# Kernel tuning notes

Measured on AMD Instinct MI355X. Metric: run time of the kernel, lower is better.

Reference implementation:

```python
import jax, jax.numpy as jnp
import numpy as np

B, CIN, H, W = 16, 1024, 32, 32
WIDTH = 256          # bottleneck width = planes * base_width/64 * cardinality
OUT = 1024           # planes * expansion
HEADS = WIDTH // 8   # 32
KS = 3               # kernel_size of SelfAttLayer


def unfold3x3(x):
    # x: (B, C, H, W) -> (B, C, 9, H, W), torch.nn.Unfold(3, padding=1) ordering (row-major kernel)
    xp = jnp.pad(x, ((0, 0), (0, 0), (1, 1), (1, 1)))
    h, w = x.shape[2], x.shape[3]
    patches = [xp[:, :, i:i + h, j:j + w] for i in range(KS) for j in range(KS)]
    return jnp.stack(patches, axis=2)


def bn(x, s, b):
    # inference-mode BatchNorm2d with running stats folded into per-channel scale/bias
    return x * s[None, :, None, None] + b[None, :, None, None]


def conv1x1(x, w):
    # w: (Cout, Cin)
    return jnp.einsum('bchw,oc->bohw', x, w)


def setup_inputs() -> dict:
    key = jax.random.key(0)
    ks = jax.random.split(key, 16)
    f = lambda k, shp, scale: (jax.random.normal(k, shp, dtype=jnp.float32) * scale)
    inp = {
        'x': f(ks[0], (B, CIN, H, W), 1.0),
        'w_conv1': f(ks[1], (WIDTH, CIN), 1.0 / np.sqrt(CIN)),
        'bn1_s': jnp.ones((WIDTH,), jnp.float32), 'bn1_b': jnp.zeros((WIDTH,), jnp.float32),
        'wq': f(ks[2], (WIDTH, WIDTH), 1.0 / np.sqrt(WIDTH)),
        'bnq_s': jnp.ones((WIDTH,), jnp.float32), 'bnq_b': jnp.zeros((WIDTH,), jnp.float32),
        'wk': f(ks[3], (WIDTH, WIDTH), 1.0 / np.sqrt(WIDTH)),
        'bnk_s': jnp.ones((WIDTH,), jnp.float32), 'bnk_b': jnp.zeros((WIDTH,), jnp.float32),
        'wv': f(ks[4], (WIDTH, WIDTH), 1.0 / np.sqrt(WIDTH)),
        'bnv_s': jnp.ones((WIDTH,), jnp.float32), 'bnv_b': jnp.zeros((WIDTH,), jnp.float32),
        'pos_h': f(ks[5], (WIDTH, KS, 1), 1.0),
        'pos_w': f(ks[6], (WIDTH, 1, KS), 1.0),
        'bnatt_s': jnp.ones((WIDTH,), jnp.float32), 'bnatt_b': jnp.zeros((WIDTH,), jnp.float32),
        'w_conv3': f(ks[7], (OUT, WIDTH), 1.0 / np.sqrt(WIDTH)),
        'bn3_s': jnp.ones((OUT,), jnp.float32), 'bn3_b': jnp.zeros((OUT,), jnp.float32),
    }
    return inp


def self_att(x, wq, bnq_s, bnq_b, wk, bnk_s, bnk_b, wv, bnv_s, bnv_b,
             pos_h, pos_w, bnatt_s, bnatt_b):
    b, c, h, w = x.shape
    d = c // HEADS
    q = jax.nn.relu(bn(conv1x1(x, wq), bnq_s, bnq_b))          # (B,C,H,W)
    k = jax.nn.relu(bn(conv1x1(x, wk), bnk_s, bnk_b))          # key_ks=1 -> 1x1 conv
    v = bn(conv1x1(x, wv), bnv_s, bnv_b)
    unfold_k = unfold3x3(k)                                     # (B,C,9,H,W)
    pos = (pos_h + pos_w).reshape(1, c, KS * KS, 1, 1)          # (1,C,9,1,1)
    kp = (unfold_k + pos).reshape(b, HEADS, d, KS * KS, h, w)
    qh = q.reshape(b, HEADS, d, h, w)
    attn = jnp.einsum('bgdhw,bgdkhw->bgkhw', qh, kp)            # (B,heads,9,H,W)
    attn = jax.nn.softmax(attn, axis=2)
    # local conv: each channel-group of size d shares its head's attention weights
    v_unf = unfold3x3(v).reshape(b, HEADS, d, KS * KS, h, w)
    out = jnp.einsum('bgdkhw,bgkhw->bgdhw', v_unf, attn).reshape(b, c, h, w)
    return jax.nn.relu(bn(out, bnatt_s, bnatt_b))


def reference(x, w_conv1, bn1_s, bn1_b, wq, bnq_s, bnq_b, wk, bnk_s, bnk_b,
              wv, bnv_s, bnv_b, pos_h, pos_w, bnatt_s, bnatt_b,
              w_conv3, bn3_s, bn3_b):
    residual = x
    h = jax.nn.relu(bn(conv1x1(x, w_conv1), bn1_s, bn1_b))
    h = self_att(h, wq, bnq_s, bnq_b, wk, bnk_s, bnk_b, wv, bnv_s, bnv_b,
                 pos_h, pos_w, bnatt_s, bnatt_b)
    h = bn(conv1x1(h, w_conv3), bn3_s, bn3_b)
    return jax.nn.relu(h + residual)
```

## Files before the change

### kernel.cpp

```cpp
#include <hip/hip_runtime.h>
#include <stdint.h>


typedef __attribute__((ext_vector_type(4))) float f32x4;
typedef __attribute__((ext_vector_type(8))) __bf16 bf16x8;
typedef __attribute__((ext_vector_type(4))) unsigned short u16x4;
typedef __attribute__((ext_vector_type(8))) unsigned short u16x8;

__device__ __forceinline__ float bf2f(unsigned short u) {
  union { unsigned int i; float f; } c; c.i = ((unsigned int)u) << 16; return c.f;
}
__device__ __forceinline__ unsigned short f2bf(float f) {
  union { float f; unsigned int i; } c; c.f = f;
  unsigned int x = c.i;
  return (unsigned short)((x + 0x7FFFu + ((x >> 16) & 1u)) >> 16);
}

__global__ __launch_bounds__(256) void k_transpose_x(const float* __restrict__ x,
                                                     unsigned short* __restrict__ xt) {
  __shared__ float tile[32][33];
  const int b  = blockIdx.z;
  const int c0 = blockIdx.y * 32;
  const int p0 = blockIdx.x * 32;
  const int tx = threadIdx.x & 31;
  const int ty = threadIdx.x >> 5;
  const float* xb = x + (size_t)b * 1048576;
  unsigned short* xtb = xt + (size_t)b * 1048576;
#pragma unroll
  for (int i = 0; i < 4; ++i)
    tile[ty + i * 8][tx] = xb[(size_t)(c0 + ty + i * 8) * 1024 + p0 + tx];
  __syncthreads();
#pragma unroll
  for (int i = 0; i < 4; ++i)
    xtb[(size_t)(p0 + ty + i * 8) * 1024 + c0 + tx] = f2bf(tile[tx][ty + i * 8]);
}

__global__ __launch_bounds__(256, 4) void k_gemm_stream(
    const float* __restrict__ A, const unsigned short* __restrict__ B,
    unsigned short* __restrict__ Cout, const float* __restrict__ scale,
    const float* __restrict__ bias, int K) {
  __shared__ unsigned short lA[2][64 * 32];
  __shared__ unsigned short lB[2][64 * 32];
  const int m0  = blockIdx.y * 64;
  const int n0  = blockIdx.x * 64;
  const int tid = threadIdx.x;
  const int lane = tid & 63;
  const int wid  = tid >> 6;
  const int wm = (wid >> 1) * 32, wn = (wid & 1) * 32;
  const int fr = lane & 15, fq = lane >> 4;

  f32x4 acc[2][2] = {};

  const int r = tid >> 2;
  const int g = tid & 3;
  const float*          Ag = A + (size_t)(m0 + r) * K + g * 8;
  const unsigned short* Bg = B + (size_t)(n0 + r) * K + g * 8;
  const int lofs = r * 32 + (g ^ (r & 3)) * 8;

  f32x4 aA[2], aB[2];
  u16x8 bvA, bvB;
  aA[0] = *(const f32x4*)(Ag);      aA[1] = *(const f32x4*)(Ag + 4);
  bvA   = *(const u16x8*)(Bg);
  aB[0] = *(const f32x4*)(Ag + 32); aB[1] = *(const f32x4*)(Ag + 36);
  bvB   = *(const u16x8*)(Bg + 32);

  int p = 0;
  for (int k0 = 0; k0 < K; k0 += 32, p ^= 1) {
    u16x8 ap;
#pragma unroll
    for (int i = 0; i < 8; ++i) ap[i] = f2bf(aA[i >> 2][i & 3]);
    *(u16x8*)&lA[p][lofs] = ap;
    *(u16x8*)&lB[p][lofs] = bvA;
    aA[0] = aB[0]; aA[1] = aB[1]; bvA = bvB;
    if (k0 + 64 < K) {
      aB[0] = *(const f32x4*)(Ag + k0 + 64);
      aB[1] = *(const f32x4*)(Ag + k0 + 68);
      bvB   = *(const u16x8*)(Bg + k0 + 64);
    }
    __syncthreads();

    bf16x8 af[2], bb[2];
#pragma unroll
    for (int i = 0; i < 2; ++i) {
      const int row = wm + i * 16 + fr;
      af[i] = *(const bf16x8*)&lA[p][row * 32 + (fq ^ (row & 3)) * 8];
    }
#pragma unroll
    for (int j = 0; j < 2; ++j) {
      const int row = wn + j * 16 + fr;
      bb[j] = *(const bf16x8*)&lB[p][row * 32 + (fq ^ (row & 3)) * 8];
    }
#pragma unroll
    for (int i = 0; i < 2; ++i)
#pragma unroll
      for (int j = 0; j < 2; ++j)
        acc[i][j] = __builtin_amdgcn_mfma_f32_16x16x32_bf16(af[i], bb[j], acc[i][j], 0, 0, 0);
  }

#pragma unroll
  for (int i = 0; i < 2; ++i) {
    const int ob = m0 + wm + i * 16 + fq * 4;
    const f32x4 s4 = *(const f32x4*)&scale[ob];
    const f32x4 b4 = *(const f32x4*)&bias[ob];
#pragma unroll
    for (int j = 0; j < 2; ++j) {
      const int P = n0 + wn + j * 16 + fr;
      u16x4 pk;
#pragma unroll
      for (int rr = 0; rr < 4; ++rr) {
        float v = fmaxf(acc[i][j][rr] * s4[rr] + b4[rr], 0.0f);
        pk[rr] = f2bf(v);
      }
      *(u16x4*)&Cout[(size_t)P * 256 + ob] = pk;
    }
  }
}

template <int MODE, int NT>
__global__ __launch_bounds__(256, 4) void k_gemm_k256(
    const float* __restrict__ A0, const float* __restrict__ A1,
    const float* __restrict__ A2, const unsigned short* __restrict__ B,
    void* __restrict__ CoutV,
    const float* __restrict__ s0, const float* __restrict__ s1,
    const float* __restrict__ s2, const float* __restrict__ b0,
    const float* __restrict__ b1, const float* __restrict__ b2,
    const float* __restrict__ resid) {
  __shared__ unsigned short lA[64 * 256];
  __shared__ unsigned short lB[2][64 * 32];
  const int mt = blockIdx.y;
  int seg, m_loc, do_relu;
  const float *A, *sc, *bi;
  if (MODE == 0) {
    seg = mt >> 2; m_loc = (mt & 3) * 64;
    A  = seg == 0 ? A0 : (seg == 1 ? A1 : A2);
    sc = seg == 0 ? s0 : (seg == 1 ? s1 : s2);
    bi = seg == 0 ? b0 : (seg == 1 ? b1 : b2);
    do_relu = (seg < 2);
  } else {
    seg = 0; m_loc = mt * 64; A = A0; sc = s0; bi = b0; do_relu = 1;
  }
  const int tid = threadIdx.x;
  const int lane = tid & 63, wid = tid >> 6;
  const int wm = (wid >> 1) * 32, wn = (wid & 1) * 32;
  const int fr = lane & 15, fq = lane >> 4;

  {
    const int rA = tid >> 2, qd = tid & 3;
    const float* Ag = A + (size_t)(m_loc + rA) * 256 + qd * 64;
#pragma unroll
    for (int m = 0; m < 8; ++m) {
      f32x4 lo = *(const f32x4*)(Ag + m * 8);
      f32x4 hi = *(const f32x4*)(Ag + m * 8 + 4);
      u16x8 pk;
#pragma unroll
      for (int e = 0; e < 4; ++e) pk[e] = f2bf(lo[e]);
#pragma unroll
      for (int e = 0; e < 4; ++e) pk[4 + e] = f2bf(hi[e]);
      const int cg = qd * 8 + m;
      *(u16x8*)&lA[rA * 256 + (cg ^ ((rA & 7) << 2)) * 8] = pk;
    }
  }

  const int rB = tid >> 2, gB = tid & 3;
  const int lofsB = rB * 32 + (gB ^ (rB & 3)) * 8;
  const int n0_blk = blockIdx.x * NT * 64;
  const unsigned short* Bg = B + (size_t)(n0_blk + rB) * 256 + gB * 8;

  u16x8 bvA = *(const u16x8*)(Bg);
  u16x8 bvB = *(const u16x8*)(Bg + 32);
  f32x4 acc[2][2] = {};
  float rres[2][2][4];
  int p = 0;
  const int TOT = NT * 8;

  for (int s = 0; s < TOT; ++s) {
    const int k0 = (s & 7) * 32;

    if (MODE == 1 && (s & 7) == 0) {
      const int n0 = n0_blk + (s >> 3) * 64;
#pragma unroll
      for (int i = 0; i < 2; ++i) {
        const int ol = m_loc + wm + i * 16 + fq * 4;
#pragma unroll
        for (int j = 0; j < 2; ++j) {
          const int P = n0 + wn + j * 16 + fr;
          const size_t base = (size_t)(P >> 10) * 1048576 + (size_t)(P & 1023);
#pragma unroll
          for (int rr = 0; rr < 4; ++rr)
            rres[i][j][rr] = resid[base + (size_t)(ol + rr) * 1024];
        }
      }
    }

    *(u16x8*)&lB[p][lofsB] = bvA;
    bvA = bvB;
    if (s + 2 < TOT) {
      const int s2i = s + 2;
      bvB = *(const u16x8*)(Bg + (size_t)(s2i >> 3) * 16384 + (s2i & 7) * 32);
    }
    __syncthreads();

    bf16x8 af[2], bb[2];
#pragma unroll
    for (int i = 0; i < 2; ++i) {
      const int row = wm + i * 16 + fr;
      const int cg = (k0 >> 3) + fq;
      af[i] = *(const bf16x8*)&lA[row * 256 + (cg ^ ((row & 7) << 2)) * 8];
    }
#pragma unroll
    for (int j = 0; j < 2; ++j) {
      const int row = wn + j * 16 + fr;
      bb[j] = *(const bf16x8*)&lB[p][row * 32 + (fq ^ (row & 3)) * 8];
    }
#pragma unroll
    for (int i = 0; i < 2; ++i)
#pragma unroll
      for (int j = 0; j < 2; ++j)
        acc[i][j] = __builtin_amdgcn_mfma_f32_16x16x32_bf16(af[i], bb[j], acc[i][j], 0, 0, 0);
    p ^= 1;

    if ((s & 7) == 7) {
      const int n0 = n0_blk + (s >> 3) * 64;
#pragma unroll
      for (int i = 0; i < 2; ++i) {
        const int ol = m_loc + wm + i * 16 + fq * 4;
        const f32x4 s4 = *(const f32x4*)&sc[ol];
        const f32x4 b4 = *(const f32x4*)&bi[ol];
#pragma unroll
        for (int j = 0; j < 2; ++j) {
          const int P = n0 + wn + j * 16 + fr;
          if (MODE == 0) {
            unsigned short* Cout = (unsigned short*)CoutV + (size_t)seg * 4194304;
            u16x4 pk;
#pragma unroll
            for (int rr = 0; rr < 4; ++rr) {
              float v = acc[i][j][rr] * s4[rr] + b4[rr];
              if (do_relu) v = fmaxf(v, 0.0f);
              pk[rr] = f2bf(v);
            }
            *(u16x4*)&Cout[(size_t)P * 256 + ol] = pk;
          } else {
            float* Cout = (float*)CoutV;
            const size_t base = (size_t)(P >> 10) * 1048576 + (size_t)(P & 1023);
#pragma unroll
            for (int rr = 0; rr < 4; ++rr) {
              float v = acc[i][j][rr] * s4[rr] + b4[rr] + rres[i][j][rr];
              Cout[base + (size_t)(ol + rr) * 1024] = fmaxf(v, 0.0f);
            }
          }
          acc[i][j] = (f32x4){0.f, 0.f, 0.f, 0.f};
        }
      }
    }
  }
}

__global__ __launch_bounds__(256, 4) void k_attn(
    const unsigned short* __restrict__ Q, const unsigned short* __restrict__ Kb,
    const unsigned short* __restrict__ Vb, unsigned short* __restrict__ O,
    const float* __restrict__ pos_h, const float* __restrict__ pos_w,
    const float* __restrict__ bs, const float* __restrict__ bb) {
  __shared__ float ph_l[3][256];
  __shared__ float pw_l[3][256];
  {
    const int c = threadIdx.x;
#pragma unroll
    for (int i = 0; i < 3; ++i) {
      ph_l[i][c] = pos_h[c * 3 + i];
      pw_l[i][c] = pos_w[c * 3 + i];
    }
  }
  __syncthreads();
  const int tid = threadIdx.x;
  const int g = tid & 31, s = tid >> 5;
  const int P = blockIdx.x * 8 + s;
  const int b = P >> 10, pix = P & 1023;
  const int hh = pix >> 5, ww = pix & 31;
  const int c0 = g * 8;

  float qf[8];
  {
    u16x8 qv = *(const u16x8*)&Q[(size_t)P * 256 + c0];
#pragma unroll
    for (int d = 0; d < 8; ++d) qf[d] = bf2f(qv[d]);
  }
  float Ai[3], Bj[3];
#pragma unroll
  for (int i = 0; i < 3; ++i) {
    float a = 0.f, w = 0.f;
#pragma unroll
    for (int d = 0; d < 8; ++d) {
      a += qf[d] * ph_l[i][c0 + d];
      w += qf[d] * pw_l[i][c0 + d];
    }
    Ai[i] = a; Bj[i] = w;
  }

  float S[9];
  int nPs[9];
#pragma unroll
  for (int t = 0; t < 9; ++t) {
    const int di = t / 3, dj = t % 3;
    const int nh = hh + di - 1, nw = ww + dj - 1;
    float sum = Ai[di] + Bj[dj];
    int nP = -1;
    if ((unsigned)nh < 32u && (unsigned)nw < 32u) {
      nP = (b << 10) + (nh << 5) + nw;
      u16x8 kv = *(const u16x8*)&Kb[(size_t)nP * 256 + c0];
#pragma unroll
      for (int d = 0; d < 8; ++d) sum += qf[d] * bf2f(kv[d]);
    }
    nPs[t] = nP;
    S[t] = sum;
  }

  float mx = S[0];
#pragma unroll
  for (int t = 1; t < 9; ++t) mx = fmaxf(mx, S[t]);
  float e[9], tot = 0.f;
#pragma unroll
  for (int t = 0; t < 9; ++t) { e[t] = __expf(S[t] - mx); tot += e[t]; }
  const float inv = 1.0f / tot;

  float of[8] = {0.f, 0.f, 0.f, 0.f, 0.f, 0.f, 0.f, 0.f};
#pragma unroll
  for (int t = 0; t < 9; ++t) {
    if (nPs[t] >= 0) {
      u16x8 vv = *(const u16x8*)&Vb[(size_t)nPs[t] * 256 + c0];
      const float w = e[t] * inv;
#pragma unroll
      for (int d = 0; d < 8; ++d) of[d] += w * bf2f(vv[d]);
    }
  }

  u16x8 res;
#pragma unroll
  for (int d = 0; d < 8; ++d) {
    float v = of[d] * bs[c0 + d] + bb[c0 + d];
    v = fmaxf(v, 0.0f);
    res[d] = f2bf(v);
  }
  *(u16x8*)&O[(size_t)P * 256 + c0] = res;
}

extern "C" void kernel_launch(void* const* d_in, const int* in_sizes, int n_in,
                              void* d_out, int out_size, void* d_ws, size_t ws_size,
                              hipStream_t stream) {
  (void)in_sizes; (void)n_in; (void)out_size; (void)ws_size;
  const float* x       = (const float*)d_in[0];
  const float* w1      = (const float*)d_in[1];
  const float* bn1_s   = (const float*)d_in[2];
  const float* bn1_b   = (const float*)d_in[3];
  const float* wq      = (const float*)d_in[4];
  const float* bnq_s   = (const float*)d_in[5];
  const float* bnq_b   = (const float*)d_in[6];
  const float* wk      = (const float*)d_in[7];
  const float* bnk_s   = (const float*)d_in[8];
  const float* bnk_b   = (const float*)d_in[9];
  const float* wv      = (const float*)d_in[10];
  const float* bnv_s   = (const float*)d_in[11];
  const float* bnv_b   = (const float*)d_in[12];
  const float* pos_h   = (const float*)d_in[13];
  const float* pos_w   = (const float*)d_in[14];
  const float* bnatt_s = (const float*)d_in[15];
  const float* bnatt_b = (const float*)d_in[16];
  const float* w3      = (const float*)d_in[17];
  const float* bn3_s   = (const float*)d_in[18];
  const float* bn3_b   = (const float*)d_in[19];

  char* ws = (char*)d_ws;
  unsigned short* h1t = (unsigned short*)(ws);
  unsigned short* qt  = (unsigned short*)(ws + 8388608);
  unsigned short* att = h1t;
  unsigned short* xt  = (unsigned short*)d_out;

  k_transpose_x<<<dim3(32, 32, 16), dim3(256), 0, stream>>>(x, xt);

  k_gemm_stream<<<dim3(256, 4), dim3(256), 0, stream>>>(w1, xt, h1t, bn1_s, bn1_b, 1024);

  k_gemm_k256<0, 4><<<dim3(64, 12), dim3(256), 0, stream>>>(
      wq, wk, wv, h1t, qt, bnq_s, bnk_s, bnv_s, bnq_b, bnk_b, bnv_b, nullptr);

  k_attn<<<dim3(2048), dim3(256), 0, stream>>>(qt, qt + 4194304, qt + 8388608, att,
                                               pos_h, pos_w, bnatt_s, bnatt_b);

  k_gemm_k256<1, 4><<<dim3(64, 16), dim3(256), 0, stream>>>(
      w3, nullptr, nullptr, att, d_out, bn3_s, nullptr, nullptr, bn3_b, nullptr,
      nullptr, x);
}
```

Before: 114.1 us.

## Fuse input transpose into conv1 GEMM with full-M tiles per block

Removes the separate x transpose/bf16 conversion kernel and has the conv1 GEMM read fp32 x directly from NCHW layout, transposing and converting it into LDS on the fly. Each block now computes all 256 output channels for 32 pixels (512 blocks), so x is read exactly once rather than written and reread as bf16. In exchange the weight matrix is reconverted from fp32 by every block, LDS stores of B are scattered 16-bit writes, and occupancy is lowered to 2 blocks per SIMD group with larger accumulators.

Measured after the change: 139.1 us. 21.9% more time.

```diff
diff --git a/kernel.cpp b/kernel.cpp
--- a/kernel.cpp
+++ b/kernel.cpp
@@ -16,102 +16,86 @@
   return (unsigned short)((x + 0x7FFFu + ((x >> 16) & 1u)) >> 16);
 }
 
-__global__ __launch_bounds__(256) void k_transpose_x(const float* __restrict__ x,
-                                                     unsigned short* __restrict__ xt) {
-  __shared__ float tile[32][33];
-  const int b  = blockIdx.z;
-  const int c0 = blockIdx.y * 32;
-  const int p0 = blockIdx.x * 32;
-  const int tx = threadIdx.x & 31;
-  const int ty = threadIdx.x >> 5;
-  const float* xb = x + (size_t)b * 1048576;
-  unsigned short* xtb = xt + (size_t)b * 1048576;
-#pragma unroll
-  for (int i = 0; i < 4; ++i)
-    tile[ty + i * 8][tx] = xb[(size_t)(c0 + ty + i * 8) * 1024 + p0 + tx];
-  __syncthreads();
-#pragma unroll
-  for (int i = 0; i < 4; ++i)
-    xtb[(size_t)(p0 + ty + i * 8) * 1024 + c0 + tx] = f2bf(tile[tx][ty + i * 8]);
-}
-
-__global__ __launch_bounds__(256, 4) void k_gemm_stream(
-    const float* __restrict__ A, const unsigned short* __restrict__ B,
-    unsigned short* __restrict__ Cout, const float* __restrict__ scale,
-    const float* __restrict__ bias, int K) {
-  __shared__ unsigned short lA[2][64 * 32];
-  __shared__ unsigned short lB[2][64 * 32];
-  const int m0  = blockIdx.y * 64;
-  const int n0  = blockIdx.x * 64;
+__global__ __launch_bounds__(256, 2) void k_conv1_fused(
+    const float* __restrict__ x, const float* __restrict__ W,
+    unsigned short* __restrict__ H, const float* __restrict__ scale,
+    const float* __restrict__ bias) {
+  __shared__ unsigned short lA[2][256 * 32];
+  __shared__ unsigned short lB[2][32 * 32];
+  const int n0 = blockIdx.x * 32;
   const int tid = threadIdx.x;
-  const int lane = tid & 63;
-  const int wid  = tid >> 6;
-  const int wm = (wid >> 1) * 32, wn = (wid & 1) * 32;
+  const int lane = tid & 63, wid = tid >> 6;
+  const int wm = wid * 64;
   const int fr = lane & 15, fq = lane >> 4;
 
-  f32x4 acc[2][2] = {};
-
-  const int r = tid >> 2;
-  const int g = tid & 3;
-  const float*          Ag = A + (size_t)(m0 + r) * K + g * 8;
-  const unsigned short* Bg = B + (size_t)(n0 + r) * K + g * 8;
-  const int lofs = r * 32 + (g ^ (r & 3)) * 8;
-
-  f32x4 aA[2], aB[2];
-  u16x8 bvA, bvB;
-  aA[0] = *(const f32x4*)(Ag);      aA[1] = *(const f32x4*)(Ag + 4);
-  bvA   = *(const u16x8*)(Bg);
-  aB[0] = *(const f32x4*)(Ag + 32); aB[1] = *(const f32x4*)(Ag + 36);
-  bvB   = *(const u16x8*)(Bg + 32);
+  f32x4 acc[4][2] = {};
+
+  const float* Ag = W + (size_t)tid * 1024;
+  const int tc = tid >> 3, tpp = (tid & 7) * 4;
+  const size_t xbase = (size_t)(n0 >> 10) * 1048576 + (n0 & 1023);
+
+  f32x4 aw[8];
+  f32x4 bx;
+#pragma unroll
+  for (int g = 0; g < 8; ++g) aw[g] = *(const f32x4*)(Ag + g * 4);
+  bx = *(const f32x4*)&x[xbase + (size_t)tc * 1024 + tpp];
 
   int p = 0;
-  for (int k0 = 0; k0 < K; k0 += 32, p ^= 1) {
-    u16x8 ap;
-#pragma unroll
-    for (int i = 0; i < 8; ++i) ap[i] = f2bf(aA[i >> 2][i & 3]);
-    *(u16x8*)&lA[p][lofs] = ap;
-    *(u16x8*)&lB[p][lofs] = bvA;
-    aA[0] = aB[0]; aA[1] = aB[1]; bvA = bvB;
-    if (k0 + 64 < K) {
-      aB[0] = *(const f32x4*)(Ag + k0 + 64);
-      aB[1] = *(const f32x4*)(Ag + k0 + 68);
-      bvB   = *(const u16x8*)(Bg + k0 + 64);
+  for (int k0 = 0; k0 < 1024; k0 += 32, p ^= 1) {
+#pragma unroll
+    for (int g = 0; g < 4; ++g) {
+      u16x8 pk;
+#pragma unroll
+      for (int e = 0; e < 4; ++e) pk[e] = f2bf(aw[2 * g][e]);
+#pragma unroll
+      for (int e = 0; e < 4; ++e) pk[4 + e] = f2bf(aw[2 * g + 1][e]);
+      *(u16x8*)&lA[p][tid * 32 + (g ^ (tid & 3)) * 8] = pk;
+    }
+#pragma unroll
+    for (int u = 0; u < 4; ++u) {
+      const int row = tpp + u;
+      lB[p][row * 32 + ((tc >> 3) ^ (row & 3)) * 8 + (tc & 7)] = f2bf(bx[u]);
+    }
+    if (k0 + 32 < 1024) {
+#pragma unroll
+      for (int g = 0; g < 8; ++g) aw[g] = *(const f32x4*)(Ag + k0 + 32 + g * 4);
+      bx = *(const f32x4*)&x[xbase + (size_t)(k0 + 32 + tc) * 1024 + tpp];
     }
     __syncthreads();
 
-    bf16x8 af[2], bb[2];
-#pragma unroll
-    for (int i = 0; i < 2; ++i) {
+    bf16x8 af[4], bb[2];
+#pragma unroll
+    for (int i = 0; i < 4; ++i) {
       const int row = wm + i * 16 + fr;
       af[i] = *(const bf16x8*)&lA[p][row * 32 + (fq ^ (row & 3)) * 8];
     }
 #pragma unroll
     for (int j = 0; j < 2; ++j) {
-      const int row = wn + j * 16 + fr;
+      const int row = j * 16 + fr;
       bb[j] = *(const bf16x8*)&lB[p][row * 32 + (fq ^ (row & 3)) * 8];
     }
 #pragma unroll
-    for (int i = 0; i < 2; ++i)
+    for (int i = 0; i < 4; ++i)
 #pragma unroll
       for (int j = 0; j < 2; ++j)
         acc[i][j] = __builtin_amdgcn_mfma_f32_16x16x32_bf16(af[i], bb[j], acc[i][j], 0, 0, 0);
   }
 
 #pragma unroll
-  for (int i = 0; i < 2; ++i) {
-    const int ob = m0 + wm + i * 16 + fq * 4;
+  for (int i = 0; i < 4; ++i) {
+    const int ob = wm + i * 16 + fq * 4;
     const f32x4 s4 = *(const f32x4*)&scale[ob];
     const f32x4 b4 = *(const f32x4*)&bias[ob];
 #pragma unroll
     for (int j = 0; j < 2; ++j) {
-      const int P = n0 + wn + j * 16 + fr;
+      const int P = n0 + j * 16 + fr;
       u16x4 pk;
 #pragma unroll
       for (int rr = 0; rr < 4; ++rr) {
         float v = fmaxf(acc[i][j][rr] * s4[rr] + b4[rr], 0.0f);
         pk[rr] = f2bf(v);
       }
-      *(u16x4*)&Cout[(size_t)P * 256 + ob] = pk;
+      *(u16x4*)&H[(size_t)P * 256 + ob] = pk;
     }
   }
 }
@@ -372,11 +356,8 @@
   unsigned short* h1t = (unsigned short*)(ws);
   unsigned short* qt  = (unsigned short*)(ws + 8388608);
   unsigned short* att = h1t;
-  unsigned short* xt  = (unsigned short*)d_out;
-
-  k_transpose_x<<<dim3(32, 32, 16), dim3(256), 0, stream>>>(x, xt);
-
-  k_gemm_stream<<<dim3(256, 4), dim3(256), 0, stream>>>(w1, xt, h1t, bn1_s, bn1_b, 1024);
+
+  k_conv1_fused<<<dim3(512), dim3(256), 0, stream>>>(x, w1, h1t, bn1_s, bn1_b);
 
   k_gemm_k256<0, 4><<<dim3(64, 12), dim3(256), 0, stream>>>(
       wq, wk, wv, h1t, qt, bnq_s, bnk_s, bnv_s, bnq_b, bnk_b, bnv_b, nullptr);
```

## Swap GEMM stationary operand: keep activation tile resident, stream weight tiles

Applied to the files above, without the earlier changes.

The K=256 GEMM kernel now keeps a 64-column activation tile (bf16) resident in shared memory and streams 64-row weight tiles through a double buffer, looping over 4 output-channel tiles per block. Previously the weight tile was resident and activations were streamed across 4 pixel tiles. Each activation tile is now read from global memory once per 256 output channels rather than once per 64-row weight tile. The cost is that fp32 weights are re-read and converted to bf16 by every block, and the grid shape changes to 768 and 1024 blocks.

New measurement: 121.2 us. +6.2%, slower.

```diff
diff --git a/kernel.cpp b/kernel.cpp
--- a/kernel.cpp
+++ b/kernel.cpp
@@ -116,8 +116,8 @@
   }
 }
 
-template <int MODE, int NT>
-__global__ __launch_bounds__(256, 4) void k_gemm_k256(
+template <int MODE>
+__global__ __launch_bounds__(256, 4) void k_gemm_n64(
     const float* __restrict__ A0, const float* __restrict__ A1,
     const float* __restrict__ A2, const unsigned short* __restrict__ B,
     void* __restrict__ CoutV,
@@ -125,19 +125,22 @@
     const float* __restrict__ s2, const float* __restrict__ b0,
     const float* __restrict__ b1, const float* __restrict__ b2,
     const float* __restrict__ resid) {
-  __shared__ unsigned short lA[64 * 256];
-  __shared__ unsigned short lB[2][64 * 32];
-  const int mt = blockIdx.y;
-  int seg, m_loc, do_relu;
+  __shared__ unsigned short lB[64 * 256];
+  __shared__ unsigned short lA[2][64 * 32];
+  const int n0 = blockIdx.x * 64;
+  const int yy = blockIdx.y;
+  int seg, do_relu, obase;
   const float *A, *sc, *bi;
   if (MODE == 0) {
-    seg = mt >> 2; m_loc = (mt & 3) * 64;
-    A  = seg == 0 ? A0 : (seg == 1 ? A1 : A2);
-    sc = seg == 0 ? s0 : (seg == 1 ? s1 : s2);
-    bi = seg == 0 ? b0 : (seg == 1 ? b1 : b2);
-    do_relu = (seg < 2);
+    seg = yy; obase = 0;
+    A  = yy == 0 ? A0 : (yy == 1 ? A1 : A2);
+    sc = yy == 0 ? s0 : (yy == 1 ? s1 : s2);
+    bi = yy == 0 ? b0 : (yy == 1 ? b1 : b2);
+    do_relu = (yy < 2);
   } else {
-    seg = 0; m_loc = mt * 64; A = A0; sc = s0; bi = b0; do_relu = 1;
+    seg = 0; obase = yy * 256;
+    A = A0 + (size_t)yy * 65536; sc = s0 + obase; bi = b0 + obase;
+    do_relu = 1;
   }
   const int tid = threadIdx.x;
   const int lane = tid & 63, wid = tid >> 6;
@@ -145,58 +148,56 @@
   const int fr = lane & 15, fq = lane >> 4;
 
   {
-    const int rA = tid >> 2, qd = tid & 3;
-    const float* Ag = A + (size_t)(m_loc + rA) * 256 + qd * 64;
+    const int rB = tid >> 2, qd = tid & 3;
+    const unsigned short* Bg = B + (size_t)(n0 + rB) * 256;
 #pragma unroll
     for (int m = 0; m < 8; ++m) {
-      f32x4 lo = *(const f32x4*)(Ag + m * 8);
-      f32x4 hi = *(const f32x4*)(Ag + m * 8 + 4);
-      u16x8 pk;
-#pragma unroll
-      for (int e = 0; e < 4; ++e) pk[e] = f2bf(lo[e]);
-#pragma unroll
-      for (int e = 0; e < 4; ++e) pk[4 + e] = f2bf(hi[e]);
-      const int cg = qd * 8 + m;
-      *(u16x8*)&lA[rA * 256 + (cg ^ ((rA & 7) << 2)) * 8] = pk;
-    }
-  }
-
-  const int rB = tid >> 2, gB = tid & 3;
-  const int lofsB = rB * 32 + (gB ^ (rB & 3)) * 8;
-  const int n0_blk = blockIdx.x * NT * 64;
-  const unsigned short* Bg = B + (size_t)(n0_blk + rB) * 256 + gB * 8;
-
-  u16x8 bvA = *(const u16x8*)(Bg);
-  u16x8 bvB = *(const u16x8*)(Bg + 32);
+      u16x8 v = *(const u16x8*)(Bg + m * 32 + qd * 8);
+      const int cg = m * 4 + qd;
+      *(u16x8*)&lB[rB * 256 + (cg ^ ((rB & 7) << 2)) * 8] = v;
+    }
+  }
+
+  const int rA = tid >> 2, gA = tid & 3;
+  const int lofsA = rA * 32 + (gA ^ (rA & 3)) * 8;
+  const float* Ag = A + (size_t)rA * 256 + gA * 8;
+
+  f32x4 aw0 = *(const f32x4*)(Ag);
+  f32x4 aw1 = *(const f32x4*)(Ag + 4);
   f32x4 acc[2][2] = {};
   float rres[2][2][4];
   int p = 0;
-  const int TOT = NT * 8;
+  const int TOT = 4 * 8;
 
   for (int s = 0; s < TOT; ++s) {
-    const int k0 = (s & 7) * 32;
-
-    if (MODE == 1 && (s & 7) == 0) {
-      const int n0 = n0_blk + (s >> 3) * 64;
+    const int mt = s >> 3, k0s = s & 7;
+
+    if (MODE == 1 && k0s == 0) {
 #pragma unroll
       for (int i = 0; i < 2; ++i) {
-        const int ol = m_loc + wm + i * 16 + fq * 4;
+        const int og = obase + mt * 64 + wm + i * 16 + fq * 4;
 #pragma unroll
         for (int j = 0; j < 2; ++j) {
           const int P = n0 + wn + j * 16 + fr;
           const size_t base = (size_t)(P >> 10) * 1048576 + (size_t)(P & 1023);
 #pragma unroll
           for (int rr = 0; rr < 4; ++rr)
-            rres[i][j][rr] = resid[base + (size_t)(ol + rr) * 1024];
+            rres[i][j][rr] = resid[base + (size_t)(og + rr) * 1024];
         }
       }
     }
 
-    *(u16x8*)&lB[p][lofsB] = bvA;
-    bvA = bvB;
-    if (s + 2 < TOT) {
-      const int s2i = s + 2;
-      bvB = *(const u16x8*)(Bg + (size_t)(s2i >> 3) * 16384 + (s2i & 7) * 32);
+    {
+      u16x8 ap;
+#pragma unroll
+      for (int i = 0; i < 8; ++i) ap[i] = f2bf((i < 4) ? aw0[i] : aw1[i - 4]);
+      *(u16x8*)&lA[p][lofsA] = ap;
+    }
+    if (s + 1 < TOT) {
+      const int s1i = s + 1;
+      const size_t off = (size_t)((s1i >> 3) * 64) * 256 + (s1i & 7) * 32;
+      aw0 = *(const f32x4*)(Ag + off);
+      aw1 = *(const f32x4*)(Ag + off + 4);
     }
     __syncthreads();
 
@@ -204,13 +205,13 @@
 #pragma unroll
     for (int i = 0; i < 2; ++i) {
       const int row = wm + i * 16 + fr;
-      const int cg = (k0 >> 3) + fq;
-      af[i] = *(const bf16x8*)&lA[row * 256 + (cg ^ ((row & 7) << 2)) * 8];
+      af[i] = *(const bf16x8*)&lA[p][row * 32 + (fq ^ (row & 3)) * 8];
     }
 #pragma unroll
     for (int j = 0; j < 2; ++j) {
       const int row = wn + j * 16 + fr;
-      bb[j] = *(const bf16x8*)&lB[p][row * 32 + (fq ^ (row & 3)) * 8];
+      const int cg = k0s * 4 + fq;
+      bb[j] = *(const bf16x8*)&lB[row * 256 + (cg ^ ((row & 7) << 2)) * 8];
     }
 #pragma unroll
     for (int i = 0; i < 2; ++i)
@@ -219,11 +220,10 @@
         acc[i][j] = __builtin_amdgcn_mfma_f32_16x16x32_bf16(af[i], bb[j], acc[i][j], 0, 0, 0);
     p ^= 1;
 
-    if ((s & 7) == 7) {
-      const int n0 = n0_blk + (s >> 3) * 64;
+    if (k0s == 7) {
 #pragma unroll
       for (int i = 0; i < 2; ++i) {
-        const int ol = m_loc + wm + i * 16 + fq * 4;
+        const int ol = mt * 64 + wm + i * 16 + fq * 4;
         const f32x4 s4 = *(const f32x4*)&sc[ol];
         const f32x4 b4 = *(const f32x4*)&bi[ol];
 #pragma unroll
@@ -241,11 +241,12 @@
             *(u16x4*)&Cout[(size_t)P * 256 + ol] = pk;
           } else {
             float* Cout = (float*)CoutV;
+            const int og = obase + ol;
             const size_t base = (size_t)(P >> 10) * 1048576 + (size_t)(P & 1023);
 #pragma unroll
             for (int rr = 0; rr < 4; ++rr) {
               float v = acc[i][j][rr] * s4[rr] + b4[rr] + rres[i][j][rr];
-              Cout[base + (size_t)(ol + rr) * 1024] = fmaxf(v, 0.0f);
+              Cout[base + (size_t)(og + rr) * 1024] = fmaxf(v, 0.0f);
             }
           }
           acc[i][j] = (f32x4){0.f, 0.f, 0.f, 0.f};
@@ -378,13 +379,13 @@
 
   k_gemm_stream<<<dim3(256, 4), dim3(256), 0, stream>>>(w1, xt, h1t, bn1_s, bn1_b, 1024);
 
-  k_gemm_k256<0, 4><<<dim3(64, 12), dim3(256), 0, stream>>>(
+  k_gemm_n64<0><<<dim3(256, 3), dim3(256), 0, stream>>>(
       wq, wk, wv, h1t, qt, bnq_s, bnk_s, bnv_s, bnq_b, bnk_b, bnv_b, nullptr);
 
   k_attn<<<dim3(2048), dim3(256), 0, stream>>>(qt, qt + 4194304, qt + 8388608, att,
                                                pos_h, pos_w, bnatt_s, bnatt_b);
 
-  k_gemm_k256<1, 4><<<dim3(64, 16), dim3(256), 0, stream>>>(
+  k_gemm_n64<1><<<dim3(256, 4), dim3(256), 0, stream>>>(
       w3, nullptr, nullptr, att, d_out, bn3_s, nullptr, nullptr, bn3_b, nullptr,
       nullptr, x);
 }
```
